# Kernel optimization log

Measured on AMD Instinct MI355X. Metric: run time of the kernel, lower is better.

## Reference

```python
import jax, jax.numpy as jnp
import numpy as np
from math import sqrt

B, S, E = 1, 2048, 1024
H, D = 16, 1024          # num_heads, d_model
DH = D // H              # head_dim = 64
EPS = 1e-5
LAMBDA_INIT = 0.8


def setup_inputs() -> dict:
    key = jax.random.key(0)
    ks = jax.random.split(key, 16)
    sd = 0.02
    x = jax.random.normal(ks[0], (B, S, E), dtype=jnp.float32)
    # causal mask: True => masked (matches torch masked_fill semantics)
    mask = jnp.triu(jnp.ones((S, S), dtype=bool), k=1)
    # per-head projection params stacked over heads: W [H, DH, E], b [H, DH]
    mk = lambda k: jax.random.normal(k, (H, DH, E), dtype=jnp.float32) * sd
    bk = lambda k: jax.random.normal(k, (H, DH), dtype=jnp.float32) * sd
    return {
        "x": x, "mask": mask,
        "Wq1": mk(ks[1]), "bq1": bk(ks[2]),
        "Wq2": mk(ks[3]), "bq2": bk(ks[4]),
        "Wk1": mk(ks[5]), "bk1": bk(ks[6]),
        "Wk2": mk(ks[7]), "bk2": bk(ks[8]),
        "Wv": mk(ks[9]), "bv": bk(ks[10]),
        "lam": jnp.full((H,), LAMBDA_INIT, dtype=jnp.float32),
        "gn_w": jnp.ones((D,), dtype=jnp.float32),
        "gn_b": jnp.zeros((D,), dtype=jnp.float32),
        "Wo": jax.random.normal(ks[11], (E, D), dtype=jnp.float32) * sd,
        "bo": jax.random.normal(ks[12], (E,), dtype=jnp.float32) * sd,
    }


def reference(x, mask, Wq1, bq1, Wq2, bq2, Wk1, bk1, Wk2, bk2, Wv, bv,
              lam, gn_w, gn_b, Wo, bo):
    scale = 1.0 / sqrt(DH)
    proj = lambda W, b: jnp.einsum('bse,hde->bhsd', x, W) + b[None, :, None, :]
    q1, q2 = proj(Wq1, bq1), proj(Wq2, bq2)
    k1, k2 = proj(Wk1, bk1), proj(Wk2, bk2)
    v = proj(Wv, bv)                                   # [B,H,S,DH]

    neg_inf = jnp.float32(-jnp.inf)
    s1 = jnp.einsum('bhsd,bhtd->bhst', q1, k1) * scale  # [B,H,S,S]
    s2 = jnp.einsum('bhsd,bhtd->bhst', q2, k2) * scale
    s1 = jnp.where(mask, neg_inf, s1)
    s2 = jnp.where(mask, neg_inf, s2)
    w = jax.nn.softmax(s1, axis=-1) - lam[None, :, None, None] * jax.nn.softmax(s2, axis=-1)
    # dropout is identity in eval mode
    out = jnp.einsum('bhst,bhtd->bhsd', w, v)           # [B,H,S,DH]

    # concat heads along feature dim -> [B,S,D]
    cat = out.transpose(0, 2, 1, 3).reshape(B, S, D)
    # GroupNorm over channels with num_groups=H: normalize each (DH, S) group
    xc = cat.transpose(0, 2, 1).reshape(B, H, DH, S)    # [B,H,DH,S]
    mu = xc.mean(axis=(2, 3), keepdims=True)
    var = xc.var(axis=(2, 3), keepdims=True)
    xn = ((xc - mu) * jax.lax.rsqrt(var + EPS)).reshape(B, D, S)
    xn = xn * gn_w[None, :, None] + gn_b[None, :, None]
    xn = xn.transpose(0, 2, 1)                          # [B,S,D]

    return xn @ Wo.T + bo                               # [B,S,E]
```

## Files before the change

kernel.cpp:

```cpp
#include <hip/hip_runtime.h>

#define S_LEN 2048
#define E_DIM 1024
#define NH 16
#define DHD 64
#define DMODEL 1024

typedef unsigned short u16;
typedef __attribute__((ext_vector_type(8))) short bf16x8;
typedef __attribute__((ext_vector_type(4))) float f32x4;

static constexpr float GN_EPS = 1e-5f;
static constexpr float QSCALE_LOG2E = 0.125f * 1.44269504088896340736f;

struct alignas(8) U16x4 { u16 x, y, z, w; };

__device__ __forceinline__ u16 f2bf(float f) {
    union { float f; unsigned u; } v; v.f = f;
    unsigned r = v.u + 0x7fffu + ((v.u >> 16) & 1u);
    return (u16)(r >> 16);
}
__device__ __forceinline__ u16 f2bf_trunc(float f) {
    union { float f; unsigned u; } v; v.f = f;
    return (u16)(v.u >> 16);
}
__device__ __forceinline__ float bf2f(u16 u) {
    union { unsigned u; float f; } v; v.u = ((unsigned)u) << 16; return v.f;
}

__device__ __forceinline__ f32x4 fzero() { f32x4 z = {0.f, 0.f, 0.f, 0.f}; return z; }

__device__ __forceinline__ void async16(const u16* g, u16* l) {
    __builtin_amdgcn_global_load_lds(
        (const __attribute__((address_space(1))) unsigned int*)g,
        (__attribute__((address_space(3))) unsigned int*)l, 16, 0, 0);
}

__device__ __forceinline__ void stage8(const u16* gbase, int gstride, u16* lds,
                                       int r0, int l) {
    const int cg = (l & 7) ^ (l >> 3);
    async16(gbase + (size_t)(r0 + (l >> 3)) * gstride + cg * 8, lds + r0 * 64);
}

__device__ __forceinline__ bf16x8 ldsfrag(const u16* lds, int r, int chunk) {
    return *(const bf16x8*)((const char*)lds + r * 128 + ((chunk ^ (r & 7)) << 4));
}

__global__ __launch_bounds__(256) void f2b_kernel(
    const float* __restrict__ x,
    const float* __restrict__ w0, const float* __restrict__ w1,
    const float* __restrict__ w2, const float* __restrict__ w3,
    const float* __restrict__ w4, const float* __restrict__ wo,
    u16* __restrict__ xb, u16* __restrict__ wall, u16* __restrict__ dwo)
{
    const int z = blockIdx.z;
    const float* src; u16* dst; int n;
    const int nw = NH * DHD * E_DIM;
    switch (z) {
        case 0: src = x;  dst = xb;            n = S_LEN * E_DIM;  break;
        case 1: src = w0; dst = wall;          n = nw; break;
        case 2: src = w1; dst = wall + nw;     n = nw; break;
        case 3: src = w2; dst = wall + 2 * nw; n = nw; break;
        case 4: src = w3; dst = wall + 3 * nw; n = nw; break;
        case 5: src = w4; dst = wall + 4 * nw; n = nw; break;
        default: src = wo; dst = dwo;          n = DMODEL * E_DIM; break;
    }
    int i = blockIdx.x * 256 + threadIdx.x;
    if (i * 4 < n) {
        float4 v = ((const float4*)src)[i];
        U16x4 o;
        o.x = f2bf(v.x); o.y = f2bf(v.y); o.z = f2bf(v.z); o.w = f2bf(v.w);
        ((U16x4*)dst)[i] = o;
    }
}

__global__ __launch_bounds__(256) void proj_mfma_kernel(
    const u16* __restrict__ xb, const u16* __restrict__ wall,
    const float* __restrict__ bq1, const float* __restrict__ bq2,
    const float* __restrict__ bk1, const float* __restrict__ bk2,
    const float* __restrict__ bv,
    u16* __restrict__ qk, u16* __restrict__ vt)
{
    __shared__ u16 As[128 * 64], Bs[128 * 64];
    const int m0 = blockIdx.x * 128, n0 = blockIdx.y * 128;
    const int t = threadIdx.x, w = t >> 6, l = t & 63;
    const int lane15 = l & 15, quad = l >> 4;
    const int wr = (w >> 1) * 64, wc = (w & 1) * 64;

    f32x4 acc[4][4];
    #pragma unroll
    for (int mi = 0; mi < 4; ++mi)
        #pragma unroll
        for (int ni = 0; ni < 4; ++ni) acc[mi][ni] = fzero();

    const u16* Ag = xb + (size_t)m0 * E_DIM;
    const u16* Bg = wall + (size_t)n0 * E_DIM;

    for (int k0 = 0; k0 < E_DIM; k0 += 64) {
        __syncthreads();
        #pragma unroll
        for (int i = 0; i < 4; ++i) stage8(Ag + k0, E_DIM, As, w * 32 + i * 8, l);
        #pragma unroll
        for (int i = 0; i < 4; ++i) stage8(Bg + k0, E_DIM, Bs, w * 32 + i * 8, l);
        __syncthreads();

        bf16x8 a[4][2], b[4][2];
        #pragma unroll
        for (int mi = 0; mi < 4; ++mi) {
            a[mi][0] = ldsfrag(As, wr + mi * 16 + lane15, quad);
            a[mi][1] = ldsfrag(As, wr + mi * 16 + lane15, 4 + quad);
        }
        #pragma unroll
        for (int ni = 0; ni < 4; ++ni) {
            b[ni][0] = ldsfrag(Bs, wc + ni * 16 + lane15, quad);
            b[ni][1] = ldsfrag(Bs, wc + ni * 16 + lane15, 4 + quad);
        }
        #pragma unroll
        for (int mi = 0; mi < 4; ++mi)
            #pragma unroll
            for (int ni = 0; ni < 4; ++ni) {
                acc[mi][ni] = __builtin_amdgcn_mfma_f32_16x16x32_bf16(
                    a[mi][0], b[ni][0], acc[mi][ni], 0, 0, 0);
                acc[mi][ni] = __builtin_amdgcn_mfma_f32_16x16x32_bf16(
                    a[mi][1], b[ni][1], acc[mi][ni], 0, 0, 0);
            }
    }

    const int tid = n0 >> 10;
    const float* bias = (tid == 0) ? bq1 : (tid == 1) ? bq2 :
                        (tid == 2) ? bk1 : (tid == 3) ? bk2 : bv;
    const float scl = (tid <= 1) ? QSCALE_LOG2E : 1.0f;
    const size_t nQKV = (size_t)NH * S_LEN * DHD;

    #pragma unroll
    for (int ni = 0; ni < 4; ++ni) {
        const int n = n0 + wc + ni * 16 + lane15;
        const int h = (n >> 6) & 15, d = n & 63;
        const float bb = bias[n & 1023];
        #pragma unroll
        for (int mi = 0; mi < 4; ++mi) {
            const int m = m0 + wr + mi * 16 + quad * 4;
            if (tid < 4) {
                u16* o = qk + tid * nQKV + ((size_t)h * S_LEN + m) * DHD + d;
                #pragma unroll
                for (int r = 0; r < 4; ++r)
                    o[r * DHD] = f2bf((acc[mi][ni][r] + bb) * scl);
            } else {
                U16x4 pk;
                pk.x = f2bf(acc[mi][ni][0] + bb);
                pk.y = f2bf(acc[mi][ni][1] + bb);
                pk.z = f2bf(acc[mi][ni][2] + bb);
                pk.w = f2bf(acc[mi][ni][3] + bb);
                *(U16x4*)(vt + ((size_t)h * DHD + d) * S_LEN + m) = pk;
            }
        }
    }
}

__global__ __launch_bounds__(256) void attn_mfma_kernel(
    const u16* __restrict__ qbase, const u16* __restrict__ kbase,
    const u16* __restrict__ vtb, u16* __restrict__ obase)
{
    __shared__ u16 Ks[3][64 * 64], Vs[3][64 * 64];
    __shared__ u16 Ps[4][16 * 64];
    const int z = blockIdx.z, h = blockIdx.y, bb = blockIdx.x;
    const size_t per = (size_t)NH * S_LEN * DHD;
    const u16* qg = qbase + z * per + (size_t)h * S_LEN * DHD;
    const u16* kg = kbase + z * per + (size_t)h * S_LEN * DHD;
    const u16* vg = vtb + (size_t)h * DHD * S_LEN;
    u16* og = obase + z * per + (size_t)h * S_LEN * DHD;
    const int t = threadIdx.x, w = t >> 6, l = t & 63;
    const int lane15 = l & 15, quad = l >> 4;
    u16* Pw = Ps[w];

    for (int half = 0; half < 2; ++half) {
        const int qt = half ? (31 - bb) : bb;
        const int q0 = qt * 64;

        const u16* qrow = qg + (size_t)(q0 + w * 16 + lane15) * DHD + quad * 8;
        bf16x8 qa0 = *(const bf16x8*)(qrow);
        bf16x8 qa1 = *(const bf16x8*)(qrow + 32);

        stage8(kg, DHD, Ks[0], w * 16, l);
        stage8(kg, DHD, Ks[0], w * 16 + 8, l);
        stage8(vg, S_LEN, Vs[0], w * 16, l);
        stage8(vg, S_LEN, Vs[0], w * 16 + 8, l);
        if (qt >= 1) {
            stage8(kg + (size_t)64 * DHD, DHD, Ks[1], w * 16, l);
            stage8(kg + (size_t)64 * DHD, DHD, Ks[1], w * 16 + 8, l);
            stage8(vg + 64, S_LEN, Vs[1], w * 16, l);
            stage8(vg + 64, S_LEN, Vs[1], w * 16 + 8, l);
        }

        f32x4 O[4];
        float lsum[4];
        #pragma unroll
        for (int i = 0; i < 4; ++i) { O[i] = fzero(); lsum[i] = 0.f; }

        int cur = 0, pre = 2;
        for (int kt = 0; kt <= qt; ++kt) {
            if (kt < qt) asm volatile("s_waitcnt vmcnt(4)" ::: "memory");
            else         asm volatile("s_waitcnt vmcnt(0)" ::: "memory");
            asm volatile("s_barrier" ::: "memory");
            if (kt + 2 <= qt) {
                const int t2 = (kt + 2) * 64;
                stage8(kg + (size_t)t2 * DHD, DHD, Ks[pre], w * 16, l);
                stage8(kg + (size_t)t2 * DHD, DHD, Ks[pre], w * 16 + 8, l);
                stage8(vg + t2, S_LEN, Vs[pre], w * 16, l);
                stage8(vg + t2, S_LEN, Vs[pre], w * 16 + 8, l);
            }
            const u16* Kc = Ks[cur];
            const u16* Vc = Vs[cur];

            f32x4 sc[4];
            #pragma unroll
            for (int nt = 0; nt < 4; ++nt) {
                sc[nt] = fzero();
                bf16x8 b0 = ldsfrag(Kc, nt * 16 + lane15, quad);
                bf16x8 b1 = ldsfrag(Kc, nt * 16 + lane15, 4 + quad);
                sc[nt] = __builtin_amdgcn_mfma_f32_16x16x32_bf16(qa0, b0, sc[nt], 0, 0, 0);
                sc[nt] = __builtin_amdgcn_mfma_f32_16x16x32_bf16(qa1, b1, sc[nt], 0, 0, 0);
            }

            const bool diag = (kt == qt);
            #pragma unroll
            for (int r = 0; r < 4; ++r) {
                const int lr = quad * 4 + r;
                const int qrl = w * 16 + lr;
                float p0 = __builtin_amdgcn_exp2f(sc[0][r]);
                float p1 = __builtin_amdgcn_exp2f(sc[1][r]);
                float p2 = __builtin_amdgcn_exp2f(sc[2][r]);
                float p3 = __builtin_amdgcn_exp2f(sc[3][r]);
                if (diag) {
                    if (lane15      > qrl) p0 = 0.f;
                    if (16 + lane15 > qrl) p1 = 0.f;
                    if (32 + lane15 > qrl) p2 = 0.f;
                    if (48 + lane15 > qrl) p3 = 0.f;
                }
                lsum[r] += (p0 + p1) + (p2 + p3);
                const int cb = (lane15 & 7) * 2;
                const int ch = lane15 >> 3;
                char* pb = (char*)Pw + lr * 128;
                *(u16*)(pb + (((0 + ch) ^ (lr & 7)) << 4) + cb) = f2bf_trunc(p0);
                *(u16*)(pb + (((2 + ch) ^ (lr & 7)) << 4) + cb) = f2bf_trunc(p1);
                *(u16*)(pb + (((4 + ch) ^ (lr & 7)) << 4) + cb) = f2bf_trunc(p2);
                *(u16*)(pb + (((6 + ch) ^ (lr & 7)) << 4) + cb) = f2bf_trunc(p3);
            }

            bf16x8 pa0 = ldsfrag(Pw, lane15, quad);
            bf16x8 pa1 = ldsfrag(Pw, lane15, 4 + quad);
            #pragma unroll
            for (int nt = 0; nt < 4; ++nt) {
                bf16x8 v0 = ldsfrag(Vc, nt * 16 + lane15, quad);
                bf16x8 v1 = ldsfrag(Vc, nt * 16 + lane15, 4 + quad);
                O[nt] = __builtin_amdgcn_mfma_f32_16x16x32_bf16(pa0, v0, O[nt], 0, 0, 0);
                O[nt] = __builtin_amdgcn_mfma_f32_16x16x32_bf16(pa1, v1, O[nt], 0, 0, 0);
            }
            cur = (cur == 2) ? 0 : cur + 1;
            pre = (pre == 2) ? 0 : pre + 1;
        }

        float inv[4];
        #pragma unroll
        for (int r = 0; r < 4; ++r) {
            float rs = lsum[r];
            rs += __shfl_xor(rs, 1);
            rs += __shfl_xor(rs, 2);
            rs += __shfl_xor(rs, 4);
            rs += __shfl_xor(rs, 8);
            inv[r] = 1.f / rs;
        }
        u16* orow = og + (size_t)(q0 + w * 16 + quad * 4) * DHD;
        #pragma unroll
        for (int nt = 0; nt < 4; ++nt) {
            const int d = nt * 16 + lane15;
            #pragma unroll
            for (int r = 0; r < 4; ++r)
                orow[r * DHD + d] = f2bf(O[nt][r] * inv[r]);
        }
        __syncthreads();
    }
}

__global__ __launch_bounds__(256) void gn_stats_kernel(
    const u16* __restrict__ o1, const u16* __restrict__ o2,
    const float* __restrict__ lam, float* __restrict__ part)
{
    const int h = blockIdx.x, p = blockIdx.y;
    const float vlam = lam[h];
    const int chunk = S_LEN * DHD / 8;
    const size_t base = (size_t)h * (S_LEN * DHD) + (size_t)p * chunk;
    const uint4* a = (const uint4*)(o1 + base);
    const uint4* b = (const uint4*)(o2 + base);
    float s = 0.f, ss = 0.f;
    for (int i = threadIdx.x; i < chunk / 8; i += 256) {
        uint4 av = a[i], bv = b[i];
        const unsigned aw[4] = {av.x, av.y, av.z, av.w};
        const unsigned bw[4] = {bv.x, bv.y, bv.z, bv.w};
        #pragma unroll
        for (int j = 0; j < 4; ++j) {
            union { unsigned u; float f; } lo_a, hi_a, lo_b, hi_b;
            lo_a.u = aw[j] << 16; hi_a.u = aw[j] & 0xffff0000u;
            lo_b.u = bw[j] << 16; hi_b.u = bw[j] & 0xffff0000u;
            float v0 = lo_a.f - vlam * lo_b.f;
            float v1 = hi_a.f - vlam * hi_b.f;
            s += v0 + v1;
            ss += v0 * v0 + v1 * v1;
        }
    }
    #pragma unroll
    for (int d = 1; d < 64; d <<= 1) { s += __shfl_xor(s, d); ss += __shfl_xor(ss, d); }
    __shared__ float red[8];
    const int w = threadIdx.x >> 6;
    if ((threadIdx.x & 63) == 0) { red[2 * w] = s; red[2 * w + 1] = ss; }
    __syncthreads();
    if (threadIdx.x == 0) {
        float S  = (red[0] + red[2]) + (red[4] + red[6]);
        float SS = (red[1] + red[3]) + (red[5] + red[7]);
        part[(blockIdx.x * 8 + p) * 2]     = S;
        part[(blockIdx.x * 8 + p) * 2 + 1] = SS;
    }
}

__global__ __launch_bounds__(256) void gn_apply_kernel(
    const u16* __restrict__ o1, const u16* __restrict__ o2,
    const float* __restrict__ lam, const float* __restrict__ part,
    const float* __restrict__ gw, const float* __restrict__ gb,
    u16* __restrict__ xnb)
{
    const int i4 = (blockIdx.x * 256 + threadIdx.x) * 4;
    const int dh = i4 & 63;
    const int s  = (i4 >> 6) & (S_LEN - 1);
    const int h  = i4 >> 17;
    const int d  = h * DHD + dh;
    float sum = 0.f, ssum = 0.f;
    #pragma unroll
    for (int p = 0; p < 8; ++p) {
        sum  += part[(h * 8 + p) * 2];
        ssum += part[(h * 8 + p) * 2 + 1];
    }
    const float n = (float)(S_LEN * DHD);
    const float mu = sum / n;
    const float rstd = rsqrtf(ssum / n - mu * mu + GN_EPS);
    const float vlam = lam[h];
    U16x4 a = *(const U16x4*)(o1 + i4);
    U16x4 b = *(const U16x4*)(o2 + i4);
    float4 g4 = *(const float4*)(gw + d);
    float4 b4 = *(const float4*)(gb + d);
    U16x4 o;
    o.x = f2bf((bf2f(a.x) - vlam * bf2f(b.x) - mu) * rstd * g4.x + b4.x);
    o.y = f2bf((bf2f(a.y) - vlam * bf2f(b.y) - mu) * rstd * g4.y + b4.y);
    o.z = f2bf((bf2f(a.z) - vlam * bf2f(b.z) - mu) * rstd * g4.z + b4.z);
    o.w = f2bf((bf2f(a.w) - vlam * bf2f(b.w) - mu) * rstd * g4.w + b4.w);
    *(U16x4*)(xnb + (size_t)s * DMODEL + d) = o;
}

__global__ __launch_bounds__(256) void out_mfma_kernel(
    const u16* __restrict__ xnb, const u16* __restrict__ wob,
    const float* __restrict__ bo, float* __restrict__ out)
{
    __shared__ u16 As[64 * 64], Bs[64 * 64];
    const int m0 = blockIdx.x * 64, n0 = blockIdx.y * 64;
    const int t = threadIdx.x, w = t >> 6, l = t & 63;
    const int lane15 = l & 15, quad = l >> 4;
    f32x4 acc[4];
    #pragma unroll
    for (int nt = 0; nt < 4; ++nt) acc[nt] = fzero();

    const u16* Ag = xnb + (size_t)m0 * DMODEL;
    const u16* Bg = wob + (size_t)n0 * DMODEL;
    for (int k0 = 0; k0 < DMODEL; k0 += 64) {
        __syncthreads();
        stage8(Ag + k0, DMODEL, As, w * 16, l);
        stage8(Ag + k0, DMODEL, As, w * 16 + 8, l);
        stage8(Bg + k0, DMODEL, Bs, w * 16, l);
        stage8(Bg + k0, DMODEL, Bs, w * 16 + 8, l);
        __syncthreads();
        bf16x8 a0 = ldsfrag(As, w * 16 + lane15, quad);
        bf16x8 a1 = ldsfrag(As, w * 16 + lane15, 4 + quad);
        #pragma unroll
        for (int nt = 0; nt < 4; ++nt) {
            bf16x8 b0 = ldsfrag(Bs, nt * 16 + lane15, quad);
            bf16x8 b1 = ldsfrag(Bs, nt * 16 + lane15, 4 + quad);
            acc[nt] = __builtin_amdgcn_mfma_f32_16x16x32_bf16(a0, b0, acc[nt], 0, 0, 0);
            acc[nt] = __builtin_amdgcn_mfma_f32_16x16x32_bf16(a1, b1, acc[nt], 0, 0, 0);
        }
    }
    #pragma unroll
    for (int nt = 0; nt < 4; ++nt) {
        const int n = n0 + nt * 16 + lane15;
        const float bb = bo[n];
        #pragma unroll
        for (int r = 0; r < 4; ++r)
            out[(size_t)(m0 + w * 16 + quad * 4 + r) * E_DIM + n] = acc[nt][r] + bb;
    }
}

extern "C" void kernel_launch(void* const* d_in, const int* in_sizes, int n_in,
                              void* d_out, int out_size, void* d_ws, size_t ws_size,
                              hipStream_t stream)
{
    const float* x   = (const float*)d_in[0];
    const float* Wq1 = (const float*)d_in[2];
    const float* bq1 = (const float*)d_in[3];
    const float* Wq2 = (const float*)d_in[4];
    const float* bq2 = (const float*)d_in[5];
    const float* Wk1 = (const float*)d_in[6];
    const float* bk1 = (const float*)d_in[7];
    const float* Wk2 = (const float*)d_in[8];
    const float* bk2 = (const float*)d_in[9];
    const float* Wv  = (const float*)d_in[10];
    const float* bv  = (const float*)d_in[11];
    const float* lam = (const float*)d_in[12];
    const float* gw  = (const float*)d_in[13];
    const float* gb  = (const float*)d_in[14];
    const float* Wo  = (const float*)d_in[15];
    const float* bo  = (const float*)d_in[16];
    float* out = (float*)d_out;

    char* p = (char*)d_ws;
    auto take = [&](size_t bytes) { char* r = p; p += (bytes + 255) & ~(size_t)255; return r; };
    const size_t nQKV = (size_t)NH * S_LEN * DHD;

    u16* xb   = (u16*)take(2 * (size_t)S_LEN * E_DIM);
    u16* wall = (u16*)take(2 * (size_t)5 * NH * DHD * E_DIM);
    u16* wob  = (u16*)take(2 * (size_t)DMODEL * E_DIM);
    u16* qk   = (u16*)take(2 * 4 * nQKV);
    u16* vtb  = (u16*)take(2 * nQKV);
    u16* o1   = (u16*)take(2 * 2 * nQKV);
    u16* xnb  = (u16*)take(2 * (size_t)S_LEN * DMODEL);
    float* part = (float*)take(4 * 256);

    f2b_kernel<<<dim3(2048, 1, 7), 256, 0, stream>>>(
        x, Wq1, Wq2, Wk1, Wk2, Wv, Wo, xb, wall, wob);

    proj_mfma_kernel<<<dim3(16, 40), 256, 0, stream>>>(
        xb, wall, bq1, bq2, bk1, bk2, bv, qk, vtb);

    attn_mfma_kernel<<<dim3(16, NH, 2), 256, 0, stream>>>(
        qk, qk + 2 * nQKV, vtb, o1);

    gn_stats_kernel<<<dim3(NH, 8), 256, 0, stream>>>(o1, o1 + nQKV, lam, part);
    gn_apply_kernel<<<dim3((int)(nQKV / 1024)), 256, 0, stream>>>(
        o1, o1 + nQKV, lam, part, gw, gb, xnb);

    out_mfma_kernel<<<dim3(32, 16), 256, 0, stream>>>(xnb, wob, bo, out);
}
```

Measured before the change: 219.5 us.

## Double-buffer GEMM K-loops and widen attention blocks to 128 query rows

The projection and output GEMMs now use double-buffered LDS tiles, so the loads for the next K-slice are issued before computing on the current one, replacing two barriers per iteration with a single waitcnt and barrier. The attention kernel moves to 512-thread blocks covering 128 query rows with 8 waves. Each K/V tile in LDS is now shared by twice as many waves, each thread stages half as much, and causal masking is applied to the last two key tiles. The costs are more LDS per block, which may lower occupancy, and a different causal load balance across blocks.

```diff
diff --git a/kernel.cpp b/kernel.cpp
--- a/kernel.cpp
+++ b/kernel.cpp
@@ -81,7 +81,7 @@
     const float* __restrict__ bv,
     u16* __restrict__ qk, u16* __restrict__ vt)
 {
-    __shared__ u16 As[128 * 64], Bs[128 * 64];
+    __shared__ u16 As[2][128 * 64], Bs[2][128 * 64];
     const int m0 = blockIdx.x * 128, n0 = blockIdx.y * 128;
     const int t = threadIdx.x, w = t >> 6, l = t & 63;
     const int lane15 = l & 15, quad = l >> 4;
@@ -96,24 +96,31 @@
     const u16* Ag = xb + (size_t)m0 * E_DIM;
     const u16* Bg = wall + (size_t)n0 * E_DIM;
 
-    for (int k0 = 0; k0 < E_DIM; k0 += 64) {
-        __syncthreads();
-        #pragma unroll
-        for (int i = 0; i < 4; ++i) stage8(Ag + k0, E_DIM, As, w * 32 + i * 8, l);
-        #pragma unroll
-        for (int i = 0; i < 4; ++i) stage8(Bg + k0, E_DIM, Bs, w * 32 + i * 8, l);
-        __syncthreads();
+    auto stageAB = [&](int k0, int buf) {
+        #pragma unroll
+        for (int i = 0; i < 4; ++i) stage8(Ag + k0, E_DIM, As[buf], w * 32 + i * 8, l);
+        #pragma unroll
+        for (int i = 0; i < 4; ++i) stage8(Bg + k0, E_DIM, Bs[buf], w * 32 + i * 8, l);
+    };
+
+    stageAB(0, 0);
+    for (int it = 0; it < 16; ++it) {
+        asm volatile("s_waitcnt vmcnt(0)" ::: "memory");
+        asm volatile("s_barrier" ::: "memory");
+        if (it + 1 < 16) stageAB((it + 1) * 64, (it + 1) & 1);
+        const u16* Ac = As[it & 1];
+        const u16* Bc = Bs[it & 1];
 
         bf16x8 a[4][2], b[4][2];
         #pragma unroll
         for (int mi = 0; mi < 4; ++mi) {
-            a[mi][0] = ldsfrag(As, wr + mi * 16 + lane15, quad);
-            a[mi][1] = ldsfrag(As, wr + mi * 16 + lane15, 4 + quad);
+            a[mi][0] = ldsfrag(Ac, wr + mi * 16 + lane15, quad);
+            a[mi][1] = ldsfrag(Ac, wr + mi * 16 + lane15, 4 + quad);
         }
         #pragma unroll
         for (int ni = 0; ni < 4; ++ni) {
-            b[ni][0] = ldsfrag(Bs, wc + ni * 16 + lane15, quad);
-            b[ni][1] = ldsfrag(Bs, wc + ni * 16 + lane15, 4 + quad);
+            b[ni][0] = ldsfrag(Bc, wc + ni * 16 + lane15, quad);
+            b[ni][1] = ldsfrag(Bc, wc + ni * 16 + lane15, 4 + quad);
         }
         #pragma unroll
         for (int mi = 0; mi < 4; ++mi)
@@ -157,12 +164,12 @@
     }
 }
 
-__global__ __launch_bounds__(256) void attn_mfma_kernel(
+__global__ __launch_bounds__(512) void attn_mfma_kernel(
     const u16* __restrict__ qbase, const u16* __restrict__ kbase,
     const u16* __restrict__ vtb, u16* __restrict__ obase)
 {
     __shared__ u16 Ks[3][64 * 64], Vs[3][64 * 64];
-    __shared__ u16 Ps[4][16 * 64];
+    __shared__ u16 Ps[8][16 * 64];
     const int z = blockIdx.z, h = blockIdx.y, bb = blockIdx.x;
     const size_t per = (size_t)NH * S_LEN * DHD;
     const u16* qg = qbase + z * per + (size_t)h * S_LEN * DHD;
@@ -174,23 +181,18 @@
     u16* Pw = Ps[w];
 
     for (int half = 0; half < 2; ++half) {
-        const int qt = half ? (31 - bb) : bb;
-        const int q0 = qt * 64;
+        const int qt = half ? (15 - bb) : bb;
+        const int q0 = qt * 128;
+        const int nkt = 2 * qt + 2;
 
         const u16* qrow = qg + (size_t)(q0 + w * 16 + lane15) * DHD + quad * 8;
         bf16x8 qa0 = *(const bf16x8*)(qrow);
         bf16x8 qa1 = *(const bf16x8*)(qrow + 32);
 
-        stage8(kg, DHD, Ks[0], w * 16, l);
-        stage8(kg, DHD, Ks[0], w * 16 + 8, l);
-        stage8(vg, S_LEN, Vs[0], w * 16, l);
-        stage8(vg, S_LEN, Vs[0], w * 16 + 8, l);
-        if (qt >= 1) {
-            stage8(kg + (size_t)64 * DHD, DHD, Ks[1], w * 16, l);
-            stage8(kg + (size_t)64 * DHD, DHD, Ks[1], w * 16 + 8, l);
-            stage8(vg + 64, S_LEN, Vs[1], w * 16, l);
-            stage8(vg + 64, S_LEN, Vs[1], w * 16 + 8, l);
-        }
+        stage8(kg, DHD, Ks[0], w * 8, l);
+        stage8(vg, S_LEN, Vs[0], w * 8, l);
+        stage8(kg + (size_t)64 * DHD, DHD, Ks[1], w * 8, l);
+        stage8(vg + 64, S_LEN, Vs[1], w * 8, l);
 
         f32x4 O[4];
         float lsum[4];
@@ -198,16 +200,14 @@
         for (int i = 0; i < 4; ++i) { O[i] = fzero(); lsum[i] = 0.f; }
 
         int cur = 0, pre = 2;
-        for (int kt = 0; kt <= qt; ++kt) {
-            if (kt < qt) asm volatile("s_waitcnt vmcnt(4)" ::: "memory");
-            else         asm volatile("s_waitcnt vmcnt(0)" ::: "memory");
+        for (int kt = 0; kt < nkt; ++kt) {
+            if (kt + 1 < nkt) asm volatile("s_waitcnt vmcnt(2)" ::: "memory");
+            else              asm volatile("s_waitcnt vmcnt(0)" ::: "memory");
             asm volatile("s_barrier" ::: "memory");
-            if (kt + 2 <= qt) {
+            if (kt + 2 < nkt) {
                 const int t2 = (kt + 2) * 64;
-                stage8(kg + (size_t)t2 * DHD, DHD, Ks[pre], w * 16, l);
-                stage8(kg + (size_t)t2 * DHD, DHD, Ks[pre], w * 16 + 8, l);
-                stage8(vg + t2, S_LEN, Vs[pre], w * 16, l);
-                stage8(vg + t2, S_LEN, Vs[pre], w * 16 + 8, l);
+                stage8(kg + (size_t)t2 * DHD, DHD, Ks[pre], w * 8, l);
+                stage8(vg + t2, S_LEN, Vs[pre], w * 8, l);
             }
             const u16* Kc = Ks[cur];
             const u16* Vc = Vs[cur];
@@ -222,20 +222,21 @@
                 sc[nt] = __builtin_amdgcn_mfma_f32_16x16x32_bf16(qa1, b1, sc[nt], 0, 0, 0);
             }
 
-            const bool diag = (kt == qt);
+            const bool doMask = (kt + 2 >= nkt);
+            const int toff = kt * 64 - q0;
             #pragma unroll
             for (int r = 0; r < 4; ++r) {
                 const int lr = quad * 4 + r;
-                const int qrl = w * 16 + lr;
                 float p0 = __builtin_amdgcn_exp2f(sc[0][r]);
                 float p1 = __builtin_amdgcn_exp2f(sc[1][r]);
                 float p2 = __builtin_amdgcn_exp2f(sc[2][r]);
                 float p3 = __builtin_amdgcn_exp2f(sc[3][r]);
-                if (diag) {
-                    if (lane15      > qrl) p0 = 0.f;
-                    if (16 + lane15 > qrl) p1 = 0.f;
-                    if (32 + lane15 > qrl) p2 = 0.f;
-                    if (48 + lane15 > qrl) p3 = 0.f;
+                if (doMask) {
+                    const int rel = w * 16 + lr - toff;
+                    if (lane15      > rel) p0 = 0.f;
+                    if (16 + lane15 > rel) p1 = 0.f;
+                    if (32 + lane15 > rel) p2 = 0.f;
+                    if (48 + lane15 > rel) p3 = 0.f;
                 }
                 lsum[r] += (p0 + p1) + (p2 + p3);
                 const int cb = (lane15 & 7) * 2;
@@ -359,7 +360,7 @@
     const u16* __restrict__ xnb, const u16* __restrict__ wob,
     const float* __restrict__ bo, float* __restrict__ out)
 {
-    __shared__ u16 As[64 * 64], Bs[64 * 64];
+    __shared__ u16 As[2][64 * 64], Bs[2][64 * 64];
     const int m0 = blockIdx.x * 64, n0 = blockIdx.y * 64;
     const int t = threadIdx.x, w = t >> 6, l = t & 63;
     const int lane15 = l & 15, quad = l >> 4;
@@ -369,19 +370,27 @@
 
     const u16* Ag = xnb + (size_t)m0 * DMODEL;
     const u16* Bg = wob + (size_t)n0 * DMODEL;
-    for (int k0 = 0; k0 < DMODEL; k0 += 64) {
-        __syncthreads();
-        stage8(Ag + k0, DMODEL, As, w * 16, l);
-        stage8(Ag + k0, DMODEL, As, w * 16 + 8, l);
-        stage8(Bg + k0, DMODEL, Bs, w * 16, l);
-        stage8(Bg + k0, DMODEL, Bs, w * 16 + 8, l);
-        __syncthreads();
-        bf16x8 a0 = ldsfrag(As, w * 16 + lane15, quad);
-        bf16x8 a1 = ldsfrag(As, w * 16 + lane15, 4 + quad);
+
+    auto stageAB = [&](int k0, int buf) {
+        stage8(Ag + k0, DMODEL, As[buf], w * 16, l);
+        stage8(Ag + k0, DMODEL, As[buf], w * 16 + 8, l);
+        stage8(Bg + k0, DMODEL, Bs[buf], w * 16, l);
+        stage8(Bg + k0, DMODEL, Bs[buf], w * 16 + 8, l);
+    };
+
+    stageAB(0, 0);
+    for (int it = 0; it < 16; ++it) {
+        asm volatile("s_waitcnt vmcnt(0)" ::: "memory");
+        asm volatile("s_barrier" ::: "memory");
+        if (it + 1 < 16) stageAB((it + 1) * 64, (it + 1) & 1);
+        const u16* Ac = As[it & 1];
+        const u16* Bc = Bs[it & 1];
+        bf16x8 a0 = ldsfrag(Ac, w * 16 + lane15, quad);
+        bf16x8 a1 = ldsfrag(Ac, w * 16 + lane15, 4 + quad);
         #pragma unroll
         for (int nt = 0; nt < 4; ++nt) {
-            bf16x8 b0 = ldsfrag(Bs, nt * 16 + lane15, quad);
-            bf16x8 b1 = ldsfrag(Bs, nt * 16 + lane15, 4 + quad);
+            bf16x8 b0 = ldsfrag(Bc, nt * 16 + lane15, quad);
+            bf16x8 b1 = ldsfrag(Bc, nt * 16 + lane15, 4 + quad);
             acc[nt] = __builtin_amdgcn_mfma_f32_16x16x32_bf16(a0, b0, acc[nt], 0, 0, 0);
             acc[nt] = __builtin_amdgcn_mfma_f32_16x16x32_bf16(a1, b1, acc[nt], 0, 0, 0);
         }
@@ -437,7 +446,7 @@
     proj_mfma_kernel<<<dim3(16, 40), 256, 0, stream>>>(
         xb, wall, bq1, bq2, bk1, bk2, bv, qk, vtb);
 
-    attn_mfma_kernel<<<dim3(16, NH, 2), 256, 0, stream>>>(
+    attn_mfma_kernel<<<dim3(8, NH, 2), 512, 0, stream>>>(
         qk, qk + 2 * nQKV, vtb, o1);
 
     gn_stats_kernel<<<dim3(NH, 8), 256, 0, stream>>>(o1, o1 + nQKV, lam, part);
```

New measurement: 233.2 us. 1.06x slower.

## Fuse both softmax branches, GroupNorm stats and apply into attention and output GEMM

Applied to the files above, without the earlier changes.

The attention kernel now runs both differential branches in one 512-thread block: the second branch's normalized output goes through LDS and is combined with lambda inside the kernel. GroupNorm sums are accumulated with atomics into a small buffer that the f2b kernel zeroes. The normalize-and-affine step moves into the output GEMM's A-tile staging, removing the separate stats and apply kernels and their intermediate buffers. In exchange, the K/V pipeline drops from triple to double buffering with full barriers, the V tile is shared between branches, and float atomics make the statistics order-dependent.

```diff
diff --git a/kernel.cpp b/kernel.cpp
--- a/kernel.cpp
+++ b/kernel.cpp
@@ -51,7 +51,8 @@
     const float* __restrict__ w0, const float* __restrict__ w1,
     const float* __restrict__ w2, const float* __restrict__ w3,
     const float* __restrict__ w4, const float* __restrict__ wo,
-    u16* __restrict__ xb, u16* __restrict__ wall, u16* __restrict__ dwo)
+    u16* __restrict__ xb, u16* __restrict__ wall, u16* __restrict__ dwo,
+    float* __restrict__ part)
 {
     const int z = blockIdx.z;
     const float* src; u16* dst; int n;
@@ -65,6 +66,8 @@
         case 5: src = w4; dst = wall + 4 * nw; n = nw; break;
         default: src = wo; dst = dwo;          n = DMODEL * E_DIM; break;
     }
+    if (z == 6 && blockIdx.x == 0 && threadIdx.x < 32)
+        part[threadIdx.x] = 0.f;
     int i = blockIdx.x * 256 + threadIdx.x;
     if (i * 4 < n) {
         float4 v = ((const float4*)src)[i];
@@ -157,60 +160,53 @@
     }
 }
 
-__global__ __launch_bounds__(256) void attn_mfma_kernel(
-    const u16* __restrict__ qbase, const u16* __restrict__ kbase,
-    const u16* __restrict__ vtb, u16* __restrict__ obase)
+__global__ __launch_bounds__(512) void attn_mfma_kernel(
+    const u16* __restrict__ qk, const u16* __restrict__ vtb,
+    const float* __restrict__ lam,
+    u16* __restrict__ vout, float* __restrict__ part)
 {
-    __shared__ u16 Ks[3][64 * 64], Vs[3][64 * 64];
-    __shared__ u16 Ps[4][16 * 64];
-    const int z = blockIdx.z, h = blockIdx.y, bb = blockIdx.x;
-    const size_t per = (size_t)NH * S_LEN * DHD;
-    const u16* qg = qbase + z * per + (size_t)h * S_LEN * DHD;
-    const u16* kg = kbase + z * per + (size_t)h * S_LEN * DHD;
-    const u16* vg = vtb + (size_t)h * DHD * S_LEN;
-    u16* og = obase + z * per + (size_t)h * S_LEN * DHD;
+    __shared__ u16 K1s[2][64 * 64], K2s[2][64 * 64], Vs[2][64 * 64];
+    __shared__ u16 Ps[8][16 * 64];
+    const int h = blockIdx.y, bb = blockIdx.x;
+    const size_t nQKV = (size_t)NH * S_LEN * DHD;
     const int t = threadIdx.x, w = t >> 6, l = t & 63;
+    const int wz = w >> 2;
+    const int wq = w & 3;
     const int lane15 = l & 15, quad = l >> 4;
+    const u16* qg  = qk + (size_t)wz * nQKV + (size_t)h * S_LEN * DHD;
+    const u16* kg1 = qk + 2 * nQKV + (size_t)h * S_LEN * DHD;
+    const u16* kg2 = kg1 + nQKV;
+    const u16* vg  = vtb + (size_t)h * DHD * S_LEN;
     u16* Pw = Ps[w];
+    const float vlam = lam[h];
 
     for (int half = 0; half < 2; ++half) {
         const int qt = half ? (31 - bb) : bb;
         const int q0 = qt * 64;
-
-        const u16* qrow = qg + (size_t)(q0 + w * 16 + lane15) * DHD + quad * 8;
+        const int nkt = qt + 1;
+
+        const u16* qrow = qg + (size_t)(q0 + wq * 16 + lane15) * DHD + quad * 8;
         bf16x8 qa0 = *(const bf16x8*)(qrow);
         bf16x8 qa1 = *(const bf16x8*)(qrow + 32);
 
-        stage8(kg, DHD, Ks[0], w * 16, l);
-        stage8(kg, DHD, Ks[0], w * 16 + 8, l);
-        stage8(vg, S_LEN, Vs[0], w * 16, l);
-        stage8(vg, S_LEN, Vs[0], w * 16 + 8, l);
-        if (qt >= 1) {
-            stage8(kg + (size_t)64 * DHD, DHD, Ks[1], w * 16, l);
-            stage8(kg + (size_t)64 * DHD, DHD, Ks[1], w * 16 + 8, l);
-            stage8(vg + 64, S_LEN, Vs[1], w * 16, l);
-            stage8(vg + 64, S_LEN, Vs[1], w * 16 + 8, l);
-        }
+        auto stageT = [&](int kt, int buf) {
+            const int t0 = kt * 64;
+            stage8(kg1 + (size_t)t0 * DHD, DHD, K1s[buf], w * 8, l);
+            stage8(kg2 + (size_t)t0 * DHD, DHD, K2s[buf], w * 8, l);
+            stage8(vg + t0, S_LEN, Vs[buf], w * 8, l);
+        };
+        stageT(0, 0);
 
         f32x4 O[4];
         float lsum[4];
         #pragma unroll
         for (int i = 0; i < 4; ++i) { O[i] = fzero(); lsum[i] = 0.f; }
 
-        int cur = 0, pre = 2;
-        for (int kt = 0; kt <= qt; ++kt) {
-            if (kt < qt) asm volatile("s_waitcnt vmcnt(4)" ::: "memory");
-            else         asm volatile("s_waitcnt vmcnt(0)" ::: "memory");
-            asm volatile("s_barrier" ::: "memory");
-            if (kt + 2 <= qt) {
-                const int t2 = (kt + 2) * 64;
-                stage8(kg + (size_t)t2 * DHD, DHD, Ks[pre], w * 16, l);
-                stage8(kg + (size_t)t2 * DHD, DHD, Ks[pre], w * 16 + 8, l);
-                stage8(vg + t2, S_LEN, Vs[pre], w * 16, l);
-                stage8(vg + t2, S_LEN, Vs[pre], w * 16 + 8, l);
-            }
-            const u16* Kc = Ks[cur];
-            const u16* Vc = Vs[cur];
+        for (int kt = 0; kt < nkt; ++kt) {
+            __syncthreads();
+            if (kt + 1 < nkt) stageT(kt + 1, (kt + 1) & 1);
+            const u16* Kc = (wz ? K2s : K1s)[kt & 1];
+            const u16* Vc = Vs[kt & 1];
 
             f32x4 sc[4];
             #pragma unroll
@@ -226,7 +222,7 @@
             #pragma unroll
             for (int r = 0; r < 4; ++r) {
                 const int lr = quad * 4 + r;
-                const int qrl = w * 16 + lr;
+                const int qrl = wq * 16 + lr;
                 float p0 = __builtin_amdgcn_exp2f(sc[0][r]);
                 float p1 = __builtin_amdgcn_exp2f(sc[1][r]);
                 float p2 = __builtin_amdgcn_exp2f(sc[2][r]);
@@ -256,8 +252,6 @@
                 O[nt] = __builtin_amdgcn_mfma_f32_16x16x32_bf16(pa0, v0, O[nt], 0, 0, 0);
                 O[nt] = __builtin_amdgcn_mfma_f32_16x16x32_bf16(pa1, v1, O[nt], 0, 0, 0);
             }
-            cur = (cur == 2) ? 0 : cur + 1;
-            pre = (pre == 2) ? 0 : pre + 1;
         }
 
         float inv[4];
@@ -270,94 +264,53 @@
             rs += __shfl_xor(rs, 8);
             inv[r] = 1.f / rs;
         }
-        u16* orow = og + (size_t)(q0 + w * 16 + quad * 4) * DHD;
-        #pragma unroll
-        for (int nt = 0; nt < 4; ++nt) {
-            const int d = nt * 16 + lane15;
-            #pragma unroll
-            for (int r = 0; r < 4; ++r)
-                orow[r * DHD + d] = f2bf(O[nt][r] * inv[r]);
-        }
-        __syncthreads();
-    }
-}
-
-__global__ __launch_bounds__(256) void gn_stats_kernel(
-    const u16* __restrict__ o1, const u16* __restrict__ o2,
-    const float* __restrict__ lam, float* __restrict__ part)
-{
-    const int h = blockIdx.x, p = blockIdx.y;
-    const float vlam = lam[h];
-    const int chunk = S_LEN * DHD / 8;
-    const size_t base = (size_t)h * (S_LEN * DHD) + (size_t)p * chunk;
-    const uint4* a = (const uint4*)(o1 + base);
-    const uint4* b = (const uint4*)(o2 + base);
-    float s = 0.f, ss = 0.f;
-    for (int i = threadIdx.x; i < chunk / 8; i += 256) {
-        uint4 av = a[i], bv = b[i];
-        const unsigned aw[4] = {av.x, av.y, av.z, av.w};
-        const unsigned bw[4] = {bv.x, bv.y, bv.z, bv.w};
-        #pragma unroll
-        for (int j = 0; j < 4; ++j) {
-            union { unsigned u; float f; } lo_a, hi_a, lo_b, hi_b;
-            lo_a.u = aw[j] << 16; hi_a.u = aw[j] & 0xffff0000u;
-            lo_b.u = bw[j] << 16; hi_b.u = bw[j] & 0xffff0000u;
-            float v0 = lo_a.f - vlam * lo_b.f;
-            float v1 = hi_a.f - vlam * hi_b.f;
-            s += v0 + v1;
-            ss += v0 * v0 + v1 * v1;
-        }
-    }
-    #pragma unroll
-    for (int d = 1; d < 64; d <<= 1) { s += __shfl_xor(s, d); ss += __shfl_xor(ss, d); }
-    __shared__ float red[8];
-    const int w = threadIdx.x >> 6;
-    if ((threadIdx.x & 63) == 0) { red[2 * w] = s; red[2 * w + 1] = ss; }
-    __syncthreads();
-    if (threadIdx.x == 0) {
-        float S  = (red[0] + red[2]) + (red[4] + red[6]);
-        float SS = (red[1] + red[3]) + (red[5] + red[7]);
-        part[(blockIdx.x * 8 + p) * 2]     = S;
-        part[(blockIdx.x * 8 + p) * 2 + 1] = SS;
-    }
-}
-
-__global__ __launch_bounds__(256) void gn_apply_kernel(
-    const u16* __restrict__ o1, const u16* __restrict__ o2,
-    const float* __restrict__ lam, const float* __restrict__ part,
+
+        __syncthreads();
+        if (wz == 1) {
+            #pragma unroll
+            for (int nt = 0; nt < 4; ++nt)
+                #pragma unroll
+                for (int r = 0; r < 4; ++r)
+                    Pw[(quad * 4 + r) * 64 + nt * 16 + lane15] =
+                        f2bf(O[nt][r] * inv[r]);
+        }
+        __syncthreads();
+        if (wz == 0) {
+            const u16* o2b = Ps[w + 4];
+            float psum = 0.f, psq = 0.f;
+            u16* orow = vout + (size_t)h * S_LEN * DHD
+                        + (size_t)(q0 + wq * 16 + quad * 4) * DHD;
+            #pragma unroll
+            for (int nt = 0; nt < 4; ++nt) {
+                const int d = nt * 16 + lane15;
+                #pragma unroll
+                for (int r = 0; r < 4; ++r) {
+                    float o1v = O[nt][r] * inv[r];
+                    float o2v = bf2f(o2b[(quad * 4 + r) * 64 + d]);
+                    float vv = o1v - vlam * o2v;
+                    psum += vv; psq += vv * vv;
+                    orow[r * DHD + d] = f2bf(vv);
+                }
+            }
+            #pragma unroll
+            for (int dd = 1; dd < 64; dd <<= 1) {
+                psum += __shfl_xor(psum, dd);
+                psq  += __shfl_xor(psq, dd);
+            }
+            if (l == 0) {
+                atomicAdd(&part[2 * h], psum);
+                atomicAdd(&part[2 * h + 1], psq);
+            }
+        }
+        __syncthreads();
+    }
+}
+
+__global__ __launch_bounds__(256) void out_mfma_kernel(
+    const u16* __restrict__ vbuf, const u16* __restrict__ wob,
+    const float* __restrict__ bo, const float* __restrict__ part,
     const float* __restrict__ gw, const float* __restrict__ gb,
-    u16* __restrict__ xnb)
-{
-    const int i4 = (blockIdx.x * 256 + threadIdx.x) * 4;
-    const int dh = i4 & 63;
-    const int s  = (i4 >> 6) & (S_LEN - 1);
-    const int h  = i4 >> 17;
-    const int d  = h * DHD + dh;
-    float sum = 0.f, ssum = 0.f;
-    #pragma unroll
-    for (int p = 0; p < 8; ++p) {
-        sum  += part[(h * 8 + p) * 2];
-        ssum += part[(h * 8 + p) * 2 + 1];
-    }
-    const float n = (float)(S_LEN * DHD);
-    const float mu = sum / n;
-    const float rstd = rsqrtf(ssum / n - mu * mu + GN_EPS);
-    const float vlam = lam[h];
-    U16x4 a = *(const U16x4*)(o1 + i4);
-    U16x4 b = *(const U16x4*)(o2 + i4);
-    float4 g4 = *(const float4*)(gw + d);
-    float4 b4 = *(const float4*)(gb + d);
-    U16x4 o;
-    o.x = f2bf((bf2f(a.x) - vlam * bf2f(b.x) - mu) * rstd * g4.x + b4.x);
-    o.y = f2bf((bf2f(a.y) - vlam * bf2f(b.y) - mu) * rstd * g4.y + b4.y);
-    o.z = f2bf((bf2f(a.z) - vlam * bf2f(b.z) - mu) * rstd * g4.z + b4.z);
-    o.w = f2bf((bf2f(a.w) - vlam * bf2f(b.w) - mu) * rstd * g4.w + b4.w);
-    *(U16x4*)(xnb + (size_t)s * DMODEL + d) = o;
-}
-
-__global__ __launch_bounds__(256) void out_mfma_kernel(
-    const u16* __restrict__ xnb, const u16* __restrict__ wob,
-    const float* __restrict__ bo, float* __restrict__ out)
+    float* __restrict__ out)
 {
     __shared__ u16 As[64 * 64], Bs[64 * 64];
     const int m0 = blockIdx.x * 64, n0 = blockIdx.y * 64;
@@ -367,15 +320,40 @@
     #pragma unroll
     for (int nt = 0; nt < 4; ++nt) acc[nt] = fzero();
 
-    const u16* Ag = xnb + (size_t)m0 * DMODEL;
     const u16* Bg = wob + (size_t)n0 * DMODEL;
-    for (int k0 = 0; k0 < DMODEL; k0 += 64) {
-        __syncthreads();
-        stage8(Ag + k0, DMODEL, As, w * 16, l);
-        stage8(Ag + k0, DMODEL, As, w * 16 + 8, l);
-        stage8(Bg + k0, DMODEL, Bs, w * 16, l);
-        stage8(Bg + k0, DMODEL, Bs, w * 16 + 8, l);
-        __syncthreads();
+    const float invn = 1.f / (float)(S_LEN * DHD);
+
+    for (int it = 0; it < 16; ++it) {
+        __syncthreads();
+        stage8(Bg + it * 64, DMODEL, Bs, w * 16, l);
+        stage8(Bg + it * 64, DMODEL, Bs, w * 16 + 8, l);
+        const float mu = part[2 * it] * invn;
+        const float rstd = rsqrtf(part[2 * it + 1] * invn - mu * mu + GN_EPS);
+        const u16* vh = vbuf + (size_t)it * S_LEN * DHD + (size_t)m0 * DHD;
+        #pragma unroll
+        for (int sl = 0; sl < 2; ++sl) {
+            const int slot = t + sl * 256;
+            const int row = slot >> 3, ch = slot & 7;
+            uint4 raw = *(const uint4*)(vh + row * DHD + ch * 8);
+            const int dbase = it * 64 + ch * 8;
+            unsigned outw[4];
+            const unsigned rw[4] = {raw.x, raw.y, raw.z, raw.w};
+            #pragma unroll
+            for (int j = 0; j < 4; ++j) {
+                const int d0 = dbase + 2 * j;
+                union { unsigned u; float f; } lo, hi;
+                lo.u = rw[j] << 16; hi.u = rw[j] & 0xffff0000u;
+                float A0 = rstd * gw[d0],     B0 = gb[d0]     - mu * rstd * gw[d0];
+                float A1 = rstd * gw[d0 + 1], B1 = gb[d0 + 1] - mu * rstd * gw[d0 + 1];
+                u16 x0 = f2bf(fmaf(lo.f, A0, B0));
+                u16 x1 = f2bf(fmaf(hi.f, A1, B1));
+                outw[j] = (unsigned)x0 | ((unsigned)x1 << 16);
+            }
+            *(uint4*)((char*)As + row * 128 + ((ch ^ (row & 7)) << 4)) =
+                make_uint4(outw[0], outw[1], outw[2], outw[3]);
+        }
+        __syncthreads();
+
         bf16x8 a0 = ldsfrag(As, w * 16 + lane15, quad);
         bf16x8 a1 = ldsfrag(As, w * 16 + lane15, 4 + quad);
         #pragma unroll
@@ -427,22 +405,18 @@
     u16* wob  = (u16*)take(2 * (size_t)DMODEL * E_DIM);
     u16* qk   = (u16*)take(2 * 4 * nQKV);
     u16* vtb  = (u16*)take(2 * nQKV);
-    u16* o1   = (u16*)take(2 * 2 * nQKV);
-    u16* xnb  = (u16*)take(2 * (size_t)S_LEN * DMODEL);
-    float* part = (float*)take(4 * 256);
+    u16* vbuf = (u16*)take(2 * nQKV);
+    float* part = (float*)take(4 * 32);
 
     f2b_kernel<<<dim3(2048, 1, 7), 256, 0, stream>>>(
-        x, Wq1, Wq2, Wk1, Wk2, Wv, Wo, xb, wall, wob);
+        x, Wq1, Wq2, Wk1, Wk2, Wv, Wo, xb, wall, wob, part);
 
     proj_mfma_kernel<<<dim3(16, 40), 256, 0, stream>>>(
         xb, wall, bq1, bq2, bk1, bk2, bv, qk, vtb);
 
-    attn_mfma_kernel<<<dim3(16, NH, 2), 256, 0, stream>>>(
-        qk, qk + 2 * nQKV, vtb, o1);
-
-    gn_stats_kernel<<<dim3(NH, 8), 256, 0, stream>>>(o1, o1 + nQKV, lam, part);
-    gn_apply_kernel<<<dim3((int)(nQKV / 1024)), 256, 0, stream>>>(
-        o1, o1 + nQKV, lam, part, gw, gb, xnb);
-
-    out_mfma_kernel<<<dim3(32, 16), 256, 0, stream>>>(xnb, wob, bo, out);
-}
+    attn_mfma_kernel<<<dim3(16, NH), 512, 0, stream>>>(
+        qk, vtb, lam, vbuf, part);
+
+    out_mfma_kernel<<<dim3(32, 16), 256, 0, stream>>>(
+        vbuf, wob, bo, part, gw, gb, out);
+}
```

After: 233.0 us. +6.1%, slower.

## Fuse GroupNorm apply into output projection GEMM A-tile staging

Applied to the files above, without the earlier changes.

Removes the separate gn_apply kernel and its intermediate xnb buffer. The output GEMM now reads both attention outputs directly and computes the lambda combination and GroupNorm affine per head on the fly. It writes the normalized bf16 tile into LDS with the swizzled layout. This saves one launch and a full write plus read of the normalized activations, but each A tile's normalization is repeated across the 16 N-column blocks and A now comes from two source buffers.

```diff
diff --git a/kernel.cpp b/kernel.cpp
--- a/kernel.cpp
+++ b/kernel.cpp
@@ -322,42 +322,12 @@
     }
 }
 
-__global__ __launch_bounds__(256) void gn_apply_kernel(
+__global__ __launch_bounds__(256) void out_mfma_kernel(
     const u16* __restrict__ o1, const u16* __restrict__ o2,
-    const float* __restrict__ lam, const float* __restrict__ part,
+    const u16* __restrict__ wob, const float* __restrict__ bo,
+    const float* __restrict__ part, const float* __restrict__ lam,
     const float* __restrict__ gw, const float* __restrict__ gb,
-    u16* __restrict__ xnb)
-{
-    const int i4 = (blockIdx.x * 256 + threadIdx.x) * 4;
-    const int dh = i4 & 63;
-    const int s  = (i4 >> 6) & (S_LEN - 1);
-    const int h  = i4 >> 17;
-    const int d  = h * DHD + dh;
-    float sum = 0.f, ssum = 0.f;
-    #pragma unroll
-    for (int p = 0; p < 8; ++p) {
-        sum  += part[(h * 8 + p) * 2];
-        ssum += part[(h * 8 + p) * 2 + 1];
-    }
-    const float n = (float)(S_LEN * DHD);
-    const float mu = sum / n;
-    const float rstd = rsqrtf(ssum / n - mu * mu + GN_EPS);
-    const float vlam = lam[h];
-    U16x4 a = *(const U16x4*)(o1 + i4);
-    U16x4 b = *(const U16x4*)(o2 + i4);
-    float4 g4 = *(const float4*)(gw + d);
-    float4 b4 = *(const float4*)(gb + d);
-    U16x4 o;
-    o.x = f2bf((bf2f(a.x) - vlam * bf2f(b.x) - mu) * rstd * g4.x + b4.x);
-    o.y = f2bf((bf2f(a.y) - vlam * bf2f(b.y) - mu) * rstd * g4.y + b4.y);
-    o.z = f2bf((bf2f(a.z) - vlam * bf2f(b.z) - mu) * rstd * g4.z + b4.z);
-    o.w = f2bf((bf2f(a.w) - vlam * bf2f(b.w) - mu) * rstd * g4.w + b4.w);
-    *(U16x4*)(xnb + (size_t)s * DMODEL + d) = o;
-}
-
-__global__ __launch_bounds__(256) void out_mfma_kernel(
-    const u16* __restrict__ xnb, const u16* __restrict__ wob,
-    const float* __restrict__ bo, float* __restrict__ out)
+    float* __restrict__ out)
 {
     __shared__ u16 As[64 * 64], Bs[64 * 64];
     const int m0 = blockIdx.x * 64, n0 = blockIdx.y * 64;
@@ -367,23 +337,64 @@
     #pragma unroll
     for (int nt = 0; nt < 4; ++nt) acc[nt] = fzero();
 
-    const u16* Ag = xnb + (size_t)m0 * DMODEL;
     const u16* Bg = wob + (size_t)n0 * DMODEL;
-    for (int k0 = 0; k0 < DMODEL; k0 += 64) {
+    const float invn = 1.f / (float)(S_LEN * DHD);
+
+    for (int it = 0; it < 16; ++it) {
         __syncthreads();
-        stage8(Ag + k0, DMODEL, As, w * 16, l);
-        stage8(Ag + k0, DMODEL, As, w * 16 + 8, l);
-        stage8(Bg + k0, DMODEL, Bs, w * 16, l);
-        stage8(Bg + k0, DMODEL, Bs, w * 16 + 8, l);
+        stage8(Bg + it * 64, DMODEL, Bs, w * 16, l);
+        stage8(Bg + it * 64, DMODEL, Bs, w * 16 + 8, l);
+        float sum = 0.f, ssum = 0.f;
+        #pragma unroll
+        for (int pp = 0; pp < 8; ++pp) {
+            sum  += part[(it * 8 + pp) * 2];
+            ssum += part[(it * 8 + pp) * 2 + 1];
+        }
+        const float mu = sum * invn;
+        const float rstd = rsqrtf(ssum * invn - mu * mu + GN_EPS);
+        const float vl = lam[it];
+        const u16* a1 = o1 + ((size_t)it * S_LEN + m0) * DHD;
+        const u16* a2 = o2 + ((size_t)it * S_LEN + m0) * DHD;
+        #pragma unroll
+        for (int sl = 0; sl < 2; ++sl) {
+            const int slot = t + sl * 256;
+            const int row = slot >> 3, ch = slot & 7;
+            uint4 r1 = *(const uint4*)(a1 + row * DHD + ch * 8);
+            uint4 r2 = *(const uint4*)(a2 + row * DHD + ch * 8);
+            const int db = it * 64 + ch * 8;
+            float4 g0 = *(const float4*)(gw + db), g1 = *(const float4*)(gw + db + 4);
+            float4 h0 = *(const float4*)(gb + db), h1 = *(const float4*)(gb + db + 4);
+            const float gws[8] = {g0.x, g0.y, g0.z, g0.w, g1.x, g1.y, g1.z, g1.w};
+            const float gbs[8] = {h0.x, h0.y, h0.z, h0.w, h1.x, h1.y, h1.z, h1.w};
+            const unsigned rw1[4] = {r1.x, r1.y, r1.z, r1.w};
+            const unsigned rw2[4] = {r2.x, r2.y, r2.z, r2.w};
+            unsigned outw[4];
+            #pragma unroll
+            for (int j = 0; j < 4; ++j) {
+                union { unsigned u; float f; } lo1, hi1, lo2, hi2;
+                lo1.u = rw1[j] << 16; hi1.u = rw1[j] & 0xffff0000u;
+                lo2.u = rw2[j] << 16; hi2.u = rw2[j] & 0xffff0000u;
+                float v0 = lo1.f - vl * lo2.f;
+                float v1 = hi1.f - vl * hi2.f;
+                float A0 = rstd * gws[2 * j],     B0 = gbs[2 * j]     - mu * A0;
+                float A1 = rstd * gws[2 * j + 1], B1 = gbs[2 * j + 1] - mu * A1;
+                u16 x0 = f2bf(fmaf(v0, A0, B0));
+                u16 x1 = f2bf(fmaf(v1, A1, B1));
+                outw[j] = (unsigned)x0 | ((unsigned)x1 << 16);
+            }
+            *(uint4*)((char*)As + row * 128 + ((ch ^ (row & 7)) << 4)) =
+                make_uint4(outw[0], outw[1], outw[2], outw[3]);
+        }
         __syncthreads();
+
         bf16x8 a0 = ldsfrag(As, w * 16 + lane15, quad);
-        bf16x8 a1 = ldsfrag(As, w * 16 + lane15, 4 + quad);
+        bf16x8 a1f = ldsfrag(As, w * 16 + lane15, 4 + quad);
         #pragma unroll
         for (int nt = 0; nt < 4; ++nt) {
             bf16x8 b0 = ldsfrag(Bs, nt * 16 + lane15, quad);
             bf16x8 b1 = ldsfrag(Bs, nt * 16 + lane15, 4 + quad);
             acc[nt] = __builtin_amdgcn_mfma_f32_16x16x32_bf16(a0, b0, acc[nt], 0, 0, 0);
-            acc[nt] = __builtin_amdgcn_mfma_f32_16x16x32_bf16(a1, b1, acc[nt], 0, 0, 0);
+            acc[nt] = __builtin_amdgcn_mfma_f32_16x16x32_bf16(a1f, b1, acc[nt], 0, 0, 0);
         }
     }
     #pragma unroll
@@ -428,7 +439,6 @@
     u16* qk   = (u16*)take(2 * 4 * nQKV);
     u16* vtb  = (u16*)take(2 * nQKV);
     u16* o1   = (u16*)take(2 * 2 * nQKV);
-    u16* xnb  = (u16*)take(2 * (size_t)S_LEN * DMODEL);
     float* part = (float*)take(4 * 256);
 
     f2b_kernel<<<dim3(2048, 1, 7), 256, 0, stream>>>(
@@ -441,8 +451,7 @@
         qk, qk + 2 * nQKV, vtb, o1);
 
     gn_stats_kernel<<<dim3(NH, 8), 256, 0, stream>>>(o1, o1 + nQKV, lam, part);
-    gn_apply_kernel<<<dim3((int)(nQKV / 1024)), 256, 0, stream>>>(
-        o1, o1 + nQKV, lam, part, gw, gb, xnb);
-
-    out_mfma_kernel<<<dim3(32, 16), 256, 0, stream>>>(xnb, wob, bo, out);
-}
+
+    out_mfma_kernel<<<dim3(32, 16), 256, 0, stream>>>(
+        o1, o1 + nQKV, wob, bo, part, lam, gw, gb, out);
+}
```

Result: slower. 226.5 us (+3.2%).
